# Kernel tuning notes

Measured on AMD Instinct MI355X. Metric: run time of the kernel, lower is better.

## Reference

```python
import jax, jax.numpy as jnp
import numpy as np

NEG_INF = -1e10  # finite stand-in for torch NEG_INF; safe under logaddexp
EOS = 1
BLANK = -1  # blank is the last vocab index (self.blank = -1)


def setup_inputs() -> dict:
    key = jax.random.key(0)
    k1, k2, k3 = jax.random.split(key, 3)
    T, V = 1500, 32000
    N, U = 8, 10
    ctc_beam = 2048
    ctc_prob = jax.random.normal(k1, (T, V), dtype=jnp.float32)
    g = jax.random.randint(k2, (N, U), 0, V)
    c = jax.random.randint(k3, (N * ctc_beam,), 0, V)
    return {"ctc_prob": ctc_prob, "g": g, "c": c}


def reference(ctc_prob, g, c):
    # --- constructor math ---
    logp = jax.nn.log_softmax(ctc_prob, axis=-1)  # T x V
    T, V = logp.shape
    N, U = g.shape
    NB = c.shape[0]
    ctc_beam = NB // N
    blank_lp = logp[:, BLANK]                     # T
    gamma_b_g0 = jnp.cumsum(blank_lp)             # T  (running blank logprob)
    # state after repeat_interleave(beam) along batch dim -> T x NB
    gamma_b_g = jnp.broadcast_to(gamma_b_g0[:, None], (T, NB))
    gamma_n_g = jnp.full((T, NB), NEG_INF, jnp.float32)
    ctc_score0 = jnp.zeros((NB,), jnp.float32)    # ctc_score repeated to NB

    # --- forward ---
    lp_c = logp[:, c]                             # T x NB, gathered per candidate
    glen = U - 1                                  # static
    start = max(glen, 1)
    if glen == 0:
        init_n = lp_c[0]
    else:
        init_n = jnp.full((NB,), NEG_INF, jnp.float32)
    init_b = jnp.full((NB,), NEG_INF, jnp.float32)
    score0 = init_n
    repeat = jnp.repeat(g[:, -1], ctc_beam) != c  # NB bool
    neg = jnp.float32(NEG_INF)

    def step(carry, xs):
        n_prev, b_prev, score = carry
        gb_gm1, gn_gm1, lp_c_t, lp_b_t = xs
        term = jnp.where(repeat, gn_gm1, neg)
        phi = jnp.logaddexp(gb_gm1, term)
        n_t = jnp.logaddexp(n_prev, phi) + lp_c_t
        b_t = jnp.logaddexp(b_prev, n_prev) + lp_b_t
        score = jnp.logaddexp(score, phi + lp_c_t)
        return (n_t, b_t, score), None

    xs = (
        gamma_b_g[start - 1:T - 1],                               # gamma_b_g[t-1]
        gamma_n_g[start - 1:T - 1],                               # gamma_n_g[t-1]
        lp_c[start:],                                             # ctc_prob[t, c]
        jnp.broadcast_to(blank_lp[start:, None], (T - start, NB)),  # ctc_prob[t, blank]
    )
    (_, _, score), _ = jax.lax.scan(step, (init_n, init_b, score0), xs)

    is_eos = c == EOS
    gamma_nb_g = jnp.logaddexp(gamma_b_g[-1], gamma_n_g[-1])
    score = jnp.where(is_eos, gamma_nb_g, score)
    delta_score = (score - ctc_score0).reshape(-1, ctc_beam)  # N x ctc_beam
    return delta_score
```

## Files before the change

kernel.cpp:

```cpp
#include <hip/hip_runtime.h>

#define T_DIM   1500
#define V_DIM   32000
#define V4      (V_DIM/4)
#define START_T 9
#define NB      16384
#define BLOCK   512
#define CPT     (NB/BLOCK)
#define FULL_J  15
#define TAIL_N  (V4 - FULL_J*BLOCK)
#define TAIL_BASE (FULL_J*BLOCK)
#define NEGBIG  -3.0e38f
#define EOS_ID  1

__global__ __launch_bounds__(BLOCK, 2)
void ctc_k1(const float* __restrict__ P, const int* __restrict__ cidx,
            float* __restrict__ Lws, float* __restrict__ Sblank,
            int rpc, int nchunk)
{
  __shared__ __align__(16) float row[V_DIM];
  __shared__ float red[16];
  const int tid = threadIdx.x;
  const int q   = blockIdx.x;
  const int t0  = q * rpc;
  int t_end = t0 + rpc; if (t_end > T_DIM) t_end = T_DIM;

  int   cid[CPT];
  float m[CPT], s[CPT];
#pragma unroll
  for (int k = 0; k < CPT; ++k) {
    cid[k] = cidx[k*BLOCK + tid];
    m[k] = NEGBIG; s[k] = 0.f;
  }

  const float4* __restrict__ P4 = (const float4*)P;
  float4* row4 = (float4*)row;
  const bool tailv = (tid < TAIL_N);
  float4 v[FULL_J];
  float4 vt;

  auto load_row = [&](int t) {
    const float4* rp = P4 + (long)t * V4;
#pragma unroll
    for (int j = 0; j < FULL_J; ++j) v[j] = rp[j*BLOCK + tid];
    vt = make_float4(NEGBIG, NEGBIG, NEGBIG, NEGBIG);
    if (tailv) vt = rp[TAIL_BASE + tid];
  };

  auto lse_stage = [&]() {
    float lm = NEGBIG;
#pragma unroll
    for (int j = 0; j < FULL_J; ++j)
      lm = fmaxf(lm, fmaxf(fmaxf(v[j].x, v[j].y), fmaxf(v[j].z, v[j].w)));
    lm = fmaxf(lm, fmaxf(fmaxf(vt.x, vt.y), fmaxf(vt.z, vt.w)));
    float ls = 0.f;
#pragma unroll
    for (int j = 0; j < FULL_J; ++j)
      ls += __expf(v[j].x - lm) + __expf(v[j].y - lm)
          + __expf(v[j].z - lm) + __expf(v[j].w - lm);
    ls += __expf(vt.x - lm) + __expf(vt.y - lm)
        + __expf(vt.z - lm) + __expf(vt.w - lm);
#pragma unroll
    for (int d = 1; d < 64; d <<= 1) {
      float om = __shfl_xor(lm, d);
      float os = __shfl_xor(ls, d);
      float nm = fmaxf(lm, om);
      ls = ls*__expf(lm - nm) + os*__expf(om - nm);
      lm = nm;
    }
    if ((tid & 63) == 0) { red[(tid>>6)*2] = lm; red[(tid>>6)*2 + 1] = ls; }
#pragma unroll
    for (int j = 0; j < FULL_J; ++j) row4[j*BLOCK + tid] = v[j];
    if (tailv) row4[TAIL_BASE + tid] = vt;
  };

  load_row(t0);
  lse_stage();
  __syncthreads();

  float Blocal = 0.f;
  for (int t = t0; t < t_end; ++t) {
    const bool has_next = (t + 1 < t_end);
    if (has_next) load_row(t + 1);

    float gm = red[0], gs = red[1];
#pragma unroll
    for (int w = 1; w < 8; ++w) {
      float om = red[2*w], os = red[2*w + 1];
      float nm = fmaxf(gm, om);
      gs = gs*__expf(gm - nm) + os*__expf(om - nm);
      gm = nm;
    }
    const float lse   = gm + __logf(gs);
    const float blank = row[V_DIM - 1] - lse;
    const float off   = Blocal - lse;
    if (t >= START_T) {
#pragma unroll
      for (int k = 0; k < CPT; ++k) {
        float term = off + row[cid[k]];
        float nm = fmaxf(m[k], term);
        s[k] = s[k]*__expf(m[k] - nm) + __expf(term - nm);
        m[k] = nm;
      }
    }
    Blocal += blank;
    __syncthreads();
    if (has_next) lse_stage();
    __syncthreads();
  }

#pragma unroll
  for (int k = 0; k < CPT; ++k) {
    float L = (s[k] > 0.f) ? (m[k] + __logf(s[k])) : NEGBIG;
    Lws[(long)q*NB + k*BLOCK + tid] = L;
  }
  if (tid == 0) Sblank[q] = Blocal;
}

#define K3_BLOCK 256
#define K3_CPB   128

__global__ __launch_bounds__(K3_BLOCK)
void ctc_k3(const float* __restrict__ Lws, const float* __restrict__ Sblank,
            const int* __restrict__ cidx, float* __restrict__ out, int nchunk)
{
  __shared__ float base[258];
  __shared__ float wsum[4];
  __shared__ float redm[K3_BLOCK], reds[K3_BLOCK];
  const int tid = threadIdx.x;

  float orig = (tid < nchunk) ? Sblank[tid] : 0.f;
  float x = orig;
#pragma unroll
  for (int d = 1; d < 64; d <<= 1) {
    float y = __shfl_up(x, d);
    if ((tid & 63) >= d) x += y;
  }
  if ((tid & 63) == 63) wsum[tid >> 6] = x;
  __syncthreads();
  {
    const int w = tid >> 6;
    float pre = 0.f;
    if (w > 0) pre += wsum[0];
    if (w > 1) pre += wsum[1];
    if (w > 2) pre += wsum[2];
    x += pre;
  }
  if (tid < nchunk)      base[tid] = x - orig;
  if (tid == nchunk - 1) base[nchunk] = x;
  __syncthreads();

  const int half = tid >> 7;
  const int cl   = tid & 127;
  const int i    = blockIdx.x * K3_CPB + cl;
  const int hl   = (nchunk + 1) >> 1;
  const int c0   = half * hl;
  int c1 = c0 + hl; if (c1 > nchunk) c1 = nchunk;

  float mm = NEGBIG, ss = 0.f;
#pragma unroll 4
  for (int q2 = c0; q2 < c1; ++q2) {
    float L = Lws[(long)q2*NB + i] + base[q2];
    float nm = fmaxf(mm, L);
    ss = ss*__expf(mm - nm) + __expf(L - nm);
    mm = nm;
  }
  redm[tid] = mm; reds[tid] = ss;
  __syncthreads();
  if (half == 0) {
    float om = redm[tid + 128], os = reds[tid + 128];
    float nm = fmaxf(mm, om);
    ss = ss*__expf(mm - nm) + os*__expf(om - nm);
    mm = nm;
    float sc = mm + __logf(ss);
    out[i] = (cidx[i] == EOS_ID) ? base[nchunk] : sc;
  }
}

extern "C" void kernel_launch(void* const* d_in, const int* in_sizes, int n_in,
                              void* d_out, int out_size, void* d_ws, size_t ws_size,
                              hipStream_t stream)
{
  const float* P    = (const float*)d_in[0];
  const int*   cidx = (const int*)d_in[2];
  float*       out  = (float*)d_out;

  long fit = ((long)ws_size/4 - 1024) / NB;
  int nchunk = (int)((fit < 250) ? fit : 250);
  if (nchunk < 1) nchunk = 1;
  int rpc = (T_DIM + nchunk - 1) / nchunk;
  nchunk  = (T_DIM + rpc - 1) / rpc;

  float* Lws    = (float*)d_ws;
  float* Sblank = Lws + (long)nchunk * NB;

  ctc_k1<<<dim3(nchunk), dim3(BLOCK), 0, stream>>>(P, cidx, Lws, Sblank, rpc, nchunk);
  ctc_k3<<<dim3(NB / K3_CPB), dim3(K3_BLOCK), 0, stream>>>(Lws, Sblank, cidx, out, nchunk);
}
```

Baseline: 64.60 us.

## Double-buffer row loads, widen blocks, and drop running-max tracking in gather

Row processing becomes a fully unrolled 6-row pipeline with two register buffers, so the global load of row t+2 overlaps the gather and softmax stage of earlier rows. Blocks grow to 1024 threads, halving candidates per thread. The per-candidate online log-sum-exp becomes a plain exp-sum, since offsets are non-positive log-probs within a short chunk. The cross-wave LSE combine now uses shuffles, and barriers become a lighter custom s_barrier. Chunk count and rows per chunk are fixed at 250 and 6, no longer derived from the workspace size. The trade-offs are higher register pressure from the two buffers and possible exp underflow if offsets become very negative.

```diff
diff --git a/kernel.cpp b/kernel.cpp
--- a/kernel.cpp
+++ b/kernel.cpp
@@ -2,64 +2,65 @@
 
 #define T_DIM   1500
 #define V_DIM   32000
-#define V4      (V_DIM/4)
+#define V4      8000
 #define START_T 9
 #define NB      16384
-#define BLOCK   512
+#define BLOCK   1024
 #define CPT     (NB/BLOCK)
-#define FULL_J  15
-#define TAIL_N  (V4 - FULL_J*BLOCK)
-#define TAIL_BASE (FULL_J*BLOCK)
+#define NJ      8
+#define TAIL_N  (V4 - 7*BLOCK)
+#define ROWS    6
+#define NCHUNK  250
 #define NEGBIG  -3.0e38f
 #define EOS_ID  1
 
-__global__ __launch_bounds__(BLOCK, 2)
+#define WG_BARRIER() do { \
+  asm volatile("s_waitcnt lgkmcnt(0)" ::: "memory"); \
+  __builtin_amdgcn_s_barrier(); \
+  asm volatile("" ::: "memory"); \
+} while (0)
+
+__global__ __launch_bounds__(BLOCK, 1)
 void ctc_k1(const float* __restrict__ P, const int* __restrict__ cidx,
-            float* __restrict__ Lws, float* __restrict__ Sblank,
-            int rpc, int nchunk)
+            float* __restrict__ Lws, float* __restrict__ Sblank)
 {
   __shared__ __align__(16) float row[V_DIM];
-  __shared__ float red[16];
+  __shared__ float red[32];
   const int tid = threadIdx.x;
   const int q   = blockIdx.x;
-  const int t0  = q * rpc;
-  int t_end = t0 + rpc; if (t_end > T_DIM) t_end = T_DIM;
+  const int t0  = q * ROWS;
 
   int   cid[CPT];
-  float m[CPT], s[CPT];
+  float s[CPT];
 #pragma unroll
   for (int k = 0; k < CPT; ++k) {
     cid[k] = cidx[k*BLOCK + tid];
-    m[k] = NEGBIG; s[k] = 0.f;
+    s[k] = 0.f;
   }
 
   const float4* __restrict__ P4 = (const float4*)P;
   float4* row4 = (float4*)row;
   const bool tailv = (tid < TAIL_N);
-  float4 v[FULL_J];
-  float4 vt;
 
-  auto load_row = [&](int t) {
+  float4 va[NJ], vb[NJ];
+
+  auto LOAD = [&](float4 (&v)[NJ], int t) {
     const float4* rp = P4 + (long)t * V4;
 #pragma unroll
-    for (int j = 0; j < FULL_J; ++j) v[j] = rp[j*BLOCK + tid];
-    vt = make_float4(NEGBIG, NEGBIG, NEGBIG, NEGBIG);
-    if (tailv) vt = rp[TAIL_BASE + tid];
+    for (int j = 0; j < 7; ++j) v[j] = rp[j*BLOCK + tid];
+    v[7] = tailv ? rp[7*BLOCK + tid] : make_float4(NEGBIG, NEGBIG, NEGBIG, NEGBIG);
   };
 
-  auto lse_stage = [&]() {
+  auto STAGE = [&](float4 (&v)[NJ]) {
     float lm = NEGBIG;
 #pragma unroll
-    for (int j = 0; j < FULL_J; ++j)
+    for (int j = 0; j < NJ; ++j)
       lm = fmaxf(lm, fmaxf(fmaxf(v[j].x, v[j].y), fmaxf(v[j].z, v[j].w)));
-    lm = fmaxf(lm, fmaxf(fmaxf(vt.x, vt.y), fmaxf(vt.z, vt.w)));
     float ls = 0.f;
 #pragma unroll
-    for (int j = 0; j < FULL_J; ++j)
+    for (int j = 0; j < NJ; ++j)
       ls += __expf(v[j].x - lm) + __expf(v[j].y - lm)
           + __expf(v[j].z - lm) + __expf(v[j].w - lm);
-    ls += __expf(vt.x - lm) + __expf(vt.y - lm)
-        + __expf(vt.z - lm) + __expf(vt.w - lm);
 #pragma unroll
     for (int d = 1; d < 64; d <<= 1) {
       float om = __shfl_xor(lm, d);
@@ -70,48 +71,52 @@
     }
     if ((tid & 63) == 0) { red[(tid>>6)*2] = lm; red[(tid>>6)*2 + 1] = ls; }
 #pragma unroll
-    for (int j = 0; j < FULL_J; ++j) row4[j*BLOCK + tid] = v[j];
-    if (tailv) row4[TAIL_BASE + tid] = vt;
+    for (int j = 0; j < 7; ++j) row4[j*BLOCK + tid] = v[j];
+    if (tailv) row4[7*BLOCK + tid] = v[7];
   };
 
-  load_row(t0);
-  lse_stage();
-  __syncthreads();
+  auto COMBINE = [&]() -> float {
+    const int w = tid & 15;
+    float m = red[2*w], sx = red[2*w + 1];
+#pragma unroll
+    for (int d = 1; d < 16; d <<= 1) {
+      float om = __shfl_xor(m, d);
+      float os = __shfl_xor(sx, d);
+      float nm = fmaxf(m, om);
+      sx = sx*__expf(m - nm) + os*__expf(om - nm);
+      m = nm;
+    }
+    return m + __logf(sx);
+  };
 
   float Blocal = 0.f;
-  for (int t = t0; t < t_end; ++t) {
-    const bool has_next = (t + 1 < t_end);
-    if (has_next) load_row(t + 1);
-
-    float gm = red[0], gs = red[1];
+  auto GATHER = [&](int t) {
+    const float lse   = COMBINE();
+    const float blank = row[V_DIM - 1] - lse;
+    if (t >= START_T) {
+      const float off = Blocal - lse;
 #pragma unroll
-    for (int w = 1; w < 8; ++w) {
-      float om = red[2*w], os = red[2*w + 1];
-      float nm = fmaxf(gm, om);
-      gs = gs*__expf(gm - nm) + os*__expf(om - nm);
-      gm = nm;
-    }
-    const float lse   = gm + __logf(gs);
-    const float blank = row[V_DIM - 1] - lse;
-    const float off   = Blocal - lse;
-    if (t >= START_T) {
-#pragma unroll
-      for (int k = 0; k < CPT; ++k) {
-        float term = off + row[cid[k]];
-        float nm = fmaxf(m[k], term);
-        s[k] = s[k]*__expf(m[k] - nm) + __expf(term - nm);
-        m[k] = nm;
-      }
+      for (int k = 0; k < CPT; ++k)
+        s[k] += __expf(off + row[cid[k]]);
     }
     Blocal += blank;
-    __syncthreads();
-    if (has_next) lse_stage();
-    __syncthreads();
-  }
+  };
+
+  LOAD(va, t0);
+  LOAD(vb, t0 + 1);
+  STAGE(va);
+  WG_BARRIER();
+
+  LOAD(va, t0 + 2); GATHER(t0 + 0); WG_BARRIER(); STAGE(vb); WG_BARRIER();
+  LOAD(vb, t0 + 3); GATHER(t0 + 1); WG_BARRIER(); STAGE(va); WG_BARRIER();
+  LOAD(va, t0 + 4); GATHER(t0 + 2); WG_BARRIER(); STAGE(vb); WG_BARRIER();
+  LOAD(vb, t0 + 5); GATHER(t0 + 3); WG_BARRIER(); STAGE(va); WG_BARRIER();
+                    GATHER(t0 + 4); WG_BARRIER(); STAGE(vb); WG_BARRIER();
+                    GATHER(t0 + 5);
 
 #pragma unroll
   for (int k = 0; k < CPT; ++k) {
-    float L = (s[k] > 0.f) ? (m[k] + __logf(s[k])) : NEGBIG;
+    float L = (s[k] > 0.f) ? __logf(s[k]) : NEGBIG;
     Lws[(long)q*NB + k*BLOCK + tid] = L;
   }
   if (tid == 0) Sblank[q] = Blocal;
@@ -185,15 +190,9 @@
   const int*   cidx = (const int*)d_in[2];
   float*       out  = (float*)d_out;
 
-  long fit = ((long)ws_size/4 - 1024) / NB;
-  int nchunk = (int)((fit < 250) ? fit : 250);
-  if (nchunk < 1) nchunk = 1;
-  int rpc = (T_DIM + nchunk - 1) / nchunk;
-  nchunk  = (T_DIM + rpc - 1) / rpc;
+  float* Lws    = (float*)d_ws;
+  float* Sblank = Lws + (long)NCHUNK * NB;
 
-  float* Lws    = (float*)d_ws;
-  float* Sblank = Lws + (long)nchunk * NB;
-
-  ctc_k1<<<dim3(nchunk), dim3(BLOCK), 0, stream>>>(P, cidx, Lws, Sblank, rpc, nchunk);
-  ctc_k3<<<dim3(NB / K3_CPB), dim3(K3_BLOCK), 0, stream>>>(Lws, Sblank, cidx, out, nchunk);
+  ctc_k1<<<dim3(NCHUNK), dim3(BLOCK), 0, stream>>>(P, cidx, Lws, Sblank);
+  ctc_k3<<<dim3(NB / K3_CPB), dim3(K3_BLOCK), 0, stream>>>(Lws, Sblank, cidx, out, NCHUNK);
 }
```

Measured after the change: 57.63 us. 10.8% less time.
